# Performance work log

Hardware: AMD Instinct MI355X
Metric: run time of the kernel (lower is better)

Reference implementation:

```python
import jax, jax.numpy as jnp
import numpy as np

K, T, F = 12000, 35, 7          # voxels, points-per-voxel (cfg.VOXEL_POINT_COUNT), point feature dim
B, D, H, W = 1, 10, 400, 352    # scatter grid: [batch, depth, cfg.INPUT_HEIGHT, cfg.INPUT_WIDTH]
C_OUT = 128
EPS = 1e-3                      # Keras BatchNormalization default epsilon


def setup_inputs() -> dict:
    key = jax.random.key(0)
    ks = jax.random.split(key, 20)
    # point features, with per-voxel padding (points beyond count are zero)
    feat = jax.random.normal(ks[0], (K, T, F), dtype=jnp.float32)
    counts = jax.random.randint(ks[1], (K,), 1, T + 1)
    valid = (jnp.arange(T)[None, :] < counts[:, None]).astype(jnp.float32)  # [K,T]
    feat = feat * valid[:, :, None]
    # voxel coordinates: (batch, d, h, w), in-range per dimension
    c0 = jax.random.randint(ks[2], (K,), 0, B)
    c1 = jax.random.randint(ks[3], (K,), 0, D)
    c2 = jax.random.randint(ks[4], (K,), 0, H)
    c3 = jax.random.randint(ks[5], (K,), 0, W)
    coordinate = jnp.stack([c0, c1, c2, c3], axis=1).astype(jnp.int32)  # [K,4]
    p = lambda i, shape: jax.random.normal(ks[i], shape, dtype=jnp.float32) * 0.1
    return {
        "input_feature": feat,
        "w1": p(6, (F, 16)), "b1": p(7, (16,)),
        "gamma1": 1.0 + p(8, (16,)), "beta1": p(9, (16,)),
        "mean1": p(10, (16,)), "var1": jax.random.uniform(ks[11], (16,), minval=0.5, maxval=1.5),
        "w2": p(12, (32, 64)), "b2": p(13, (64,)),
        "gamma2": 1.0 + p(14, (64,)), "beta2": p(15, (64,)),
        "mean2": p(16, (64,)), "var2": jax.random.uniform(ks[17], (64,), minval=0.5, maxval=1.5),
        "coordinate": coordinate,
        "batch_size": B,
    }


def vfe(x, mask, w, b, gamma, beta, mean, var):
    # Dense + relu (per point), inference BatchNorm, max-aggregate, tile-concat, mask
    dense = jax.nn.relu(jnp.einsum('ktf,fu->ktu', x, w) + b)
    pw = gamma * (dense - mean) * jax.lax.rsqrt(var + EPS) + beta  # [K,T,U]
    agg = jnp.max(pw, axis=1, keepdims=True)                       # [K,1,U]
    cat = jnp.concatenate([pw, jnp.broadcast_to(agg, pw.shape)], axis=2)  # [K,T,2U]
    return cat * mask


def reference(input_feature, w1, b1, gamma1, beta1, mean1, var1,
              w2, b2, gamma2, beta2, mean2, var2, coordinate, batch_size):
    # mask: point is valid if max over its features != 0
    mask = (jnp.max(input_feature, axis=2, keepdims=True) != 0).astype(input_feature.dtype)
    x = vfe(input_feature, mask, w1, b1, gamma1, beta1, mean1, var1)   # [K,T,32]
    x = vfe(x, mask, w2, b2, gamma2, beta2, mean2, var2)               # [K,T,128]
    voxelwise = jnp.max(x, axis=1)                                     # [K,128]
    out = jnp.zeros((batch_size, D, H, W, C_OUT), dtype=voxelwise.dtype)
    # tf.scatter_nd semantics: duplicate indices accumulate (add)
    out = out.at[coordinate[:, 0], coordinate[:, 1], coordinate[:, 2], coordinate[:, 3]].add(voxelwise)
    return out
```

## Files before the change

kernel.cpp:

```cpp
#include <hip/hip_runtime.h>

#define KVOX 12000
#define TPTS 35
#define FIN  7
#define DD   10
#define HH   400
#define WW   352
#define CO   128
#define EPSBN 1e-3f
#define NCELL (DD * HH * WW)
#define CELLS_PER_BLK 8

__global__ __launch_bounds__(64) void vfe_compute(
    const float* __restrict__ feat,
    const float* __restrict__ w1, const float* __restrict__ b1,
    const float* __restrict__ g1, const float* __restrict__ be1,
    const float* __restrict__ m1, const float* __restrict__ v1,
    const float* __restrict__ w2, const float* __restrict__ b2,
    const float* __restrict__ g2, const float* __restrict__ be2,
    const float* __restrict__ m2, const float* __restrict__ v2,
    const int* __restrict__ coord,
    float* __restrict__ vox,
    int* __restrict__ head,
    int* __restrict__ nxt)
{
    const int k   = blockIdx.x;
    const int tid = threadIdx.x;

    __shared__ float sx[TPTS][FIN];
    __shared__ float smask[TPTS];
    __shared__ __align__(16) float sx2[TPTS][32];

    const float* fk = feat + (size_t)k * (TPTS * FIN);
    for (int i = tid; i < TPTS * FIN; i += 64)
        ((float*)sx)[i] = fk[i];
    __syncthreads();

    bool pred = false;
    if (tid < TPTS) {
        float mx = sx[tid][0];
        #pragma unroll
        for (int f = 1; f < FIN; ++f) mx = fmaxf(mx, sx[tid][f]);
        pred = (mx != 0.0f);
        smask[tid] = pred ? 1.0f : 0.0f;
    }
    unsigned long long bal = __ballot(pred);
    const int nvalid = __popcll(bal);
    __syncthreads();

    if (tid < 16) {
        const int u = tid;
        float w1c[FIN];
        #pragma unroll
        for (int f = 0; f < FIN; ++f) w1c[f] = w1[f * 16 + u];
        const float b     = b1[u];
        const float scale = g1[u] * rsqrtf(v1[u] + EPSBN);
        const float shift = be1[u] - m1[u] * scale;

        float agg = -INFINITY;
        float pw[TPTS];
        #pragma unroll
        for (int t = 0; t < TPTS; ++t) {
            float d = b;
            #pragma unroll
            for (int f = 0; f < FIN; ++f) d = fmaf(sx[t][f], w1c[f], d);
            d = fmaxf(d, 0.0f);
            float p = fmaf(d, scale, shift);
            agg = fmaxf(agg, p);
            pw[t] = p;
        }
        #pragma unroll
        for (int t = 0; t < TPTS; ++t) {
            const float mk = smask[t];
            sx2[t][u]      = pw[t] * mk;
            sx2[t][16 + u] = agg   * mk;
        }
    }
    __syncthreads();

    {
        const int v = tid;
        float w2c[32];
        #pragma unroll
        for (int u = 0; u < 32; ++u) w2c[u] = w2[u * 64 + v];
        const float b     = b2[v];
        const float scale = g2[v] * rsqrtf(v2[v] + EPSBN);
        const float shift = be2[v] - m2[v] * scale;

        float aggAll = -INFINITY;
        float voxA   = -INFINITY;
        #pragma unroll 5
        for (int t = 0; t < TPTS; ++t) {
            float d = b;
            const float4* xr = (const float4*)(&sx2[t][0]);
            #pragma unroll
            for (int q = 0; q < 8; ++q) {
                float4 xv = xr[q];
                d = fmaf(xv.x, w2c[4 * q + 0], d);
                d = fmaf(xv.y, w2c[4 * q + 1], d);
                d = fmaf(xv.z, w2c[4 * q + 2], d);
                d = fmaf(xv.w, w2c[4 * q + 3], d);
            }
            d = fmaxf(d, 0.0f);
            float p = fmaf(d, scale, shift);
            aggAll = fmaxf(aggAll, p);
            voxA   = fmaxf(voxA, p * smask[t]);
        }
        float voxB;
        if (nvalid == 0)          voxB = 0.0f;
        else if (nvalid < TPTS)   voxB = fmaxf(aggAll, 0.0f);
        else                      voxB = aggAll;

        float* vk = vox + (size_t)k * CO;
        vk[v]      = voxA;
        vk[64 + v] = voxB;

        if (v == 0) {
            const int4 c = ((const int4*)coord)[k];
            const int loc = (((c.x * DD + c.y) * HH + c.z) * WW + c.w);
            nxt[k] = atomicExch(&head[loc], k);
        }
    }
}

__global__ __launch_bounds__(256) void gather_out(
    const float* __restrict__ vox, const int* __restrict__ head,
    const int* __restrict__ nxt, float* __restrict__ out)
{
    const int tid  = threadIdx.x;
    const int cell = blockIdx.x * CELLS_PER_BLK + (tid >> 5);
    const int lane = tid & 31;

    float4 acc = make_float4(0.f, 0.f, 0.f, 0.f);
    int s = head[cell];
    while (s >= 0) {
        const float4 v = ((const float4*)vox)[s * 32 + lane];
        acc.x += v.x; acc.y += v.y; acc.z += v.z; acc.w += v.w;
        s = nxt[s];
    }
    ((float4*)out)[(size_t)cell * 32 + lane] = acc;
}

__global__ __launch_bounds__(64) void vfe_scatter_atomic(
    const float* __restrict__ feat,
    const float* __restrict__ w1, const float* __restrict__ b1,
    const float* __restrict__ g1, const float* __restrict__ be1,
    const float* __restrict__ m1, const float* __restrict__ v1,
    const float* __restrict__ w2, const float* __restrict__ b2,
    const float* __restrict__ g2, const float* __restrict__ be2,
    const float* __restrict__ m2, const float* __restrict__ v2,
    const int* __restrict__ coord,
    float* __restrict__ out)
{
    const int k   = blockIdx.x;
    const int tid = threadIdx.x;
    __shared__ float sx[TPTS][FIN];
    __shared__ float smask[TPTS];
    __shared__ __align__(16) float sx2[TPTS][32];
    const float* fk = feat + (size_t)k * (TPTS * FIN);
    for (int i = tid; i < TPTS * FIN; i += 64) ((float*)sx)[i] = fk[i];
    __syncthreads();
    bool pred = false;
    if (tid < TPTS) {
        float mx = sx[tid][0];
        #pragma unroll
        for (int f = 1; f < FIN; ++f) mx = fmaxf(mx, sx[tid][f]);
        pred = (mx != 0.0f);
        smask[tid] = pred ? 1.0f : 0.0f;
    }
    unsigned long long bal = __ballot(pred);
    const int nvalid = __popcll(bal);
    __syncthreads();
    if (tid < 16) {
        const int u = tid;
        float w1c[FIN];
        #pragma unroll
        for (int f = 0; f < FIN; ++f) w1c[f] = w1[f * 16 + u];
        const float b = b1[u];
        const float scale = g1[u] * rsqrtf(v1[u] + EPSBN);
        const float shift = be1[u] - m1[u] * scale;
        float agg = -INFINITY;
        float pw[TPTS];
        #pragma unroll
        for (int t = 0; t < TPTS; ++t) {
            float d = b;
            #pragma unroll
            for (int f = 0; f < FIN; ++f) d = fmaf(sx[t][f], w1c[f], d);
            d = fmaxf(d, 0.0f);
            float p = fmaf(d, scale, shift);
            agg = fmaxf(agg, p);
            pw[t] = p;
        }
        #pragma unroll
        for (int t = 0; t < TPTS; ++t) {
            const float mk = smask[t];
            sx2[t][u] = pw[t] * mk;
            sx2[t][16 + u] = agg * mk;
        }
    }
    __syncthreads();
    {
        const int v = tid;
        float w2c[32];
        #pragma unroll
        for (int u = 0; u < 32; ++u) w2c[u] = w2[u * 64 + v];
        const float b = b2[v];
        const float scale = g2[v] * rsqrtf(v2[v] + EPSBN);
        const float shift = be2[v] - m2[v] * scale;
        float aggAll = -INFINITY, voxA = -INFINITY;
        #pragma unroll 5
        for (int t = 0; t < TPTS; ++t) {
            float d = b;
            const float4* xr = (const float4*)(&sx2[t][0]);
            #pragma unroll
            for (int q = 0; q < 8; ++q) {
                float4 xv = xr[q];
                d = fmaf(xv.x, w2c[4 * q + 0], d);
                d = fmaf(xv.y, w2c[4 * q + 1], d);
                d = fmaf(xv.z, w2c[4 * q + 2], d);
                d = fmaf(xv.w, w2c[4 * q + 3], d);
            }
            d = fmaxf(d, 0.0f);
            float p = fmaf(d, scale, shift);
            aggAll = fmaxf(aggAll, p);
            voxA = fmaxf(voxA, p * smask[t]);
        }
        float voxB;
        if (nvalid == 0) voxB = 0.0f;
        else if (nvalid < TPTS) voxB = fmaxf(aggAll, 0.0f);
        else voxB = aggAll;
        const int4 c = ((const int4*)coord)[k];
        const int loc = (((c.x * DD + c.y) * HH + c.z) * WW + c.w);
        float* o = out + (size_t)loc * CO;
        atomicAdd(o + v, voxA);
        atomicAdd(o + 64 + v, voxB);
    }
}

extern "C" void kernel_launch(void* const* d_in, const int* in_sizes, int n_in,
                              void* d_out, int out_size, void* d_ws, size_t ws_size,
                              hipStream_t stream) {
    const float* feat = (const float*)d_in[0];
    const float* w1   = (const float*)d_in[1];
    const float* b1   = (const float*)d_in[2];
    const float* g1   = (const float*)d_in[3];
    const float* be1  = (const float*)d_in[4];
    const float* m1   = (const float*)d_in[5];
    const float* v1   = (const float*)d_in[6];
    const float* w2   = (const float*)d_in[7];
    const float* b2   = (const float*)d_in[8];
    const float* g2   = (const float*)d_in[9];
    const float* be2  = (const float*)d_in[10];
    const float* m2   = (const float*)d_in[11];
    const float* v2   = (const float*)d_in[12];
    const int*   coord = (const int*)d_in[13];
    float* out = (float*)d_out;

    const size_t voxB  = (size_t)KVOX * CO * sizeof(float);
    const size_t headB = (size_t)NCELL * sizeof(int);
    const size_t nxtB  = (size_t)KVOX * sizeof(int);
    const size_t need  = voxB + headB + nxtB;

    if (ws_size >= need) {
        float* vox = (float*)d_ws;
        int*   head = (int*)((char*)d_ws + voxB);
        int*   nxt  = (int*)((char*)d_ws + voxB + headB);

        hipMemsetAsync(head, 0xFF, headB, stream);
        vfe_compute<<<KVOX, 64, 0, stream>>>(feat, w1, b1, g1, be1, m1, v1,
                                             w2, b2, g2, be2, m2, v2, coord,
                                             vox, head, nxt);
        gather_out<<<NCELL / CELLS_PER_BLK, 256, 0, stream>>>(vox, head, nxt, out);
    } else {
        hipMemsetAsync(d_out, 0, (size_t)out_size * sizeof(float), stream);
        vfe_scatter_atomic<<<KVOX, 64, 0, stream>>>(feat, w1, b1, g1, be1, m1, v1,
                                                    w2, b2, g2, be2, m2, v2, coord, out);
    }
}
```

Before: 795.1 us.

## Fuse output zero-fill with VFE compute and replace linked-list gather with atomic scatter

The separate head-array memset and linked-list gather pass over every output cell are removed. The output zero-fill now runs inside the VFE compute kernel, whose blocks hold four voxels each and alternate between filling before or after their compute so the fill and compute overlap. A second small kernel then scatters voxel features into the output with per-channel atomic adds. This drops the head and next workspace and the gather pass's pointer chasing, at the cost of one large 180MB fill plus atomic contention on any duplicate cells.

```diff
diff --git a/kernel.cpp b/kernel.cpp
--- a/kernel.cpp
+++ b/kernel.cpp
@@ -9,9 +9,11 @@
 #define CO   128
 #define EPSBN 1e-3f
 #define NCELL (DD * HH * WW)
-#define CELLS_PER_BLK 8
-
-__global__ __launch_bounds__(64) void vfe_compute(
+#define CB    3000
+#define TOTALF4 ((size_t)NCELL * 32)
+#define SB    1500
+
+__global__ __launch_bounds__(256) void fused_fill_compute(
     const float* __restrict__ feat,
     const float* __restrict__ w1, const float* __restrict__ b1,
     const float* __restrict__ g1, const float* __restrict__ be1,
@@ -19,126 +21,132 @@
     const float* __restrict__ w2, const float* __restrict__ b2,
     const float* __restrict__ g2, const float* __restrict__ be2,
     const float* __restrict__ m2, const float* __restrict__ v2,
-    const int* __restrict__ coord,
     float* __restrict__ vox,
-    int* __restrict__ head,
-    int* __restrict__ nxt)
-{
-    const int k   = blockIdx.x;
-    const int tid = threadIdx.x;
-
-    __shared__ float sx[TPTS][FIN];
-    __shared__ float smask[TPTS];
-    __shared__ __align__(16) float sx2[TPTS][32];
-
-    const float* fk = feat + (size_t)k * (TPTS * FIN);
-    for (int i = tid; i < TPTS * FIN; i += 64)
-        ((float*)sx)[i] = fk[i];
-    __syncthreads();
-
-    bool pred = false;
-    if (tid < TPTS) {
-        float mx = sx[tid][0];
-        #pragma unroll
-        for (int f = 1; f < FIN; ++f) mx = fmaxf(mx, sx[tid][f]);
-        pred = (mx != 0.0f);
-        smask[tid] = pred ? 1.0f : 0.0f;
-    }
-    unsigned long long bal = __ballot(pred);
-    const int nvalid = __popcll(bal);
-    __syncthreads();
-
-    if (tid < 16) {
-        const int u = tid;
-        float w1c[FIN];
-        #pragma unroll
-        for (int f = 0; f < FIN; ++f) w1c[f] = w1[f * 16 + u];
-        const float b     = b1[u];
-        const float scale = g1[u] * rsqrtf(v1[u] + EPSBN);
-        const float shift = be1[u] - m1[u] * scale;
-
-        float agg = -INFINITY;
-        float pw[TPTS];
-        #pragma unroll
-        for (int t = 0; t < TPTS; ++t) {
-            float d = b;
-            #pragma unroll
-            for (int f = 0; f < FIN; ++f) d = fmaf(sx[t][f], w1c[f], d);
-            d = fmaxf(d, 0.0f);
-            float p = fmaf(d, scale, shift);
-            agg = fmaxf(agg, p);
-            pw[t] = p;
-        }
-        #pragma unroll
-        for (int t = 0; t < TPTS; ++t) {
-            const float mk = smask[t];
-            sx2[t][u]      = pw[t] * mk;
-            sx2[t][16 + u] = agg   * mk;
-        }
-    }
-    __syncthreads();
-
-    {
-        const int v = tid;
-        float w2c[32];
-        #pragma unroll
-        for (int u = 0; u < 32; ++u) w2c[u] = w2[u * 64 + v];
-        const float b     = b2[v];
-        const float scale = g2[v] * rsqrtf(v2[v] + EPSBN);
-        const float shift = be2[v] - m2[v] * scale;
-
-        float aggAll = -INFINITY;
-        float voxA   = -INFINITY;
-        #pragma unroll 5
-        for (int t = 0; t < TPTS; ++t) {
-            float d = b;
-            const float4* xr = (const float4*)(&sx2[t][0]);
-            #pragma unroll
-            for (int q = 0; q < 8; ++q) {
-                float4 xv = xr[q];
-                d = fmaf(xv.x, w2c[4 * q + 0], d);
-                d = fmaf(xv.y, w2c[4 * q + 1], d);
-                d = fmaf(xv.z, w2c[4 * q + 2], d);
-                d = fmaf(xv.w, w2c[4 * q + 3], d);
-            }
-            d = fmaxf(d, 0.0f);
-            float p = fmaf(d, scale, shift);
-            aggAll = fmaxf(aggAll, p);
-            voxA   = fmaxf(voxA, p * smask[t]);
-        }
-        float voxB;
-        if (nvalid == 0)          voxB = 0.0f;
-        else if (nvalid < TPTS)   voxB = fmaxf(aggAll, 0.0f);
-        else                      voxB = aggAll;
-
-        float* vk = vox + (size_t)k * CO;
-        vk[v]      = voxA;
-        vk[64 + v] = voxB;
-
-        if (v == 0) {
-            const int4 c = ((const int4*)coord)[k];
-            const int loc = (((c.x * DD + c.y) * HH + c.z) * WW + c.w);
-            nxt[k] = atomicExch(&head[loc], k);
-        }
-    }
-}
-
-__global__ __launch_bounds__(256) void gather_out(
-    const float* __restrict__ vox, const int* __restrict__ head,
-    const int* __restrict__ nxt, float* __restrict__ out)
+    float* __restrict__ out)
 {
     const int tid  = threadIdx.x;
-    const int cell = blockIdx.x * CELLS_PER_BLK + (tid >> 5);
-    const int lane = tid & 31;
-
-    float4 acc = make_float4(0.f, 0.f, 0.f, 0.f);
-    int s = head[cell];
-    while (s >= 0) {
-        const float4 v = ((const float4*)vox)[s * 32 + lane];
-        acc.x += v.x; acc.y += v.y; acc.z += v.z; acc.w += v.w;
-        s = nxt[s];
-    }
-    ((float4*)out)[(size_t)cell * 32 + lane] = acc;
+    const int wv   = tid >> 6;
+    const int lane = tid & 63;
+    const int k    = blockIdx.x * 4 + wv;
+
+    __shared__ float sx[4][TPTS][FIN];
+    __shared__ float smask[4][TPTS];
+    __shared__ __align__(16) float sx2[4][TPTS][32];
+
+    const bool fillFirst = (blockIdx.x & 1);
+
+    auto do_fill = [&]() {
+        const float4 z = make_float4(0.f, 0.f, 0.f, 0.f);
+        float4* o4 = (float4*)out;
+        const size_t stride = (size_t)CB * 256;
+        for (size_t i = (size_t)blockIdx.x * 256 + tid; i < TOTALF4; i += stride)
+            o4[i] = z;
+    };
+
+    if (fillFirst) do_fill();
+
+    {
+        const float* fk = feat + (size_t)k * (TPTS * FIN);
+        for (int i = lane; i < TPTS * FIN; i += 64)
+            ((float*)sx[wv])[i] = fk[i];
+        __syncthreads();
+
+        bool pred = false;
+        if (lane < TPTS) {
+            float mx = sx[wv][lane][0];
+            #pragma unroll
+            for (int f = 1; f < FIN; ++f) mx = fmaxf(mx, sx[wv][lane][f]);
+            pred = (mx != 0.0f);
+            smask[wv][lane] = pred ? 1.0f : 0.0f;
+        }
+        unsigned long long bal = __ballot(pred);
+        const int nvalid = __popcll(bal);
+        __syncthreads();
+
+        if (lane < 16) {
+            const int u = lane;
+            float w1c[FIN];
+            #pragma unroll
+            for (int f = 0; f < FIN; ++f) w1c[f] = w1[f * 16 + u];
+            const float b     = b1[u];
+            const float scale = g1[u] * rsqrtf(v1[u] + EPSBN);
+            const float shift = be1[u] - m1[u] * scale;
+
+            float agg = -INFINITY;
+            float pw[TPTS];
+            #pragma unroll
+            for (int t = 0; t < TPTS; ++t) {
+                float d = b;
+                #pragma unroll
+                for (int f = 0; f < FIN; ++f) d = fmaf(sx[wv][t][f], w1c[f], d);
+                d = fmaxf(d, 0.0f);
+                float p = fmaf(d, scale, shift);
+                agg = fmaxf(agg, p);
+                pw[t] = p;
+            }
+            #pragma unroll
+            for (int t = 0; t < TPTS; ++t) {
+                const float mk = smask[wv][t];
+                sx2[wv][t][u]      = pw[t] * mk;
+                sx2[wv][t][16 + u] = agg   * mk;
+            }
+        }
+        __syncthreads();
+
+        {
+            const int v = lane;
+            float w2c[32];
+            #pragma unroll
+            for (int u = 0; u < 32; ++u) w2c[u] = w2[u * 64 + v];
+            const float b     = b2[v];
+            const float scale = g2[v] * rsqrtf(v2[v] + EPSBN);
+            const float shift = be2[v] - m2[v] * scale;
+
+            float aggAll = -INFINITY;
+            float voxA   = -INFINITY;
+            #pragma unroll 5
+            for (int t = 0; t < TPTS; ++t) {
+                float d = b;
+                const float4* xr = (const float4*)(&sx2[wv][t][0]);
+                #pragma unroll
+                for (int q = 0; q < 8; ++q) {
+                    float4 xv = xr[q];
+                    d = fmaf(xv.x, w2c[4 * q + 0], d);
+                    d = fmaf(xv.y, w2c[4 * q + 1], d);
+                    d = fmaf(xv.z, w2c[4 * q + 2], d);
+                    d = fmaf(xv.w, w2c[4 * q + 3], d);
+                }
+                d = fmaxf(d, 0.0f);
+                float p = fmaf(d, scale, shift);
+                aggAll = fmaxf(aggAll, p);
+                voxA   = fmaxf(voxA, p * smask[wv][t]);
+            }
+            float voxB;
+            if (nvalid == 0)          voxB = 0.0f;
+            else if (nvalid < TPTS)   voxB = fmaxf(aggAll, 0.0f);
+            else                      voxB = aggAll;
+
+            float* vk = vox + (size_t)k * CO;
+            vk[v]      = voxA;
+            vk[64 + v] = voxB;
+        }
+    }
+
+    if (!fillFirst) do_fill();
+}
+
+__global__ __launch_bounds__(256) void scatter_add(
+    const float* __restrict__ vox, const int* __restrict__ coord,
+    float* __restrict__ out)
+{
+    const int stride = SB * 256;
+    for (int i = blockIdx.x * 256 + threadIdx.x; i < KVOX * CO; i += stride) {
+        const int k  = i >> 7;
+        const int ch = i & (CO - 1);
+        const int4 c = ((const int4*)coord)[k];
+        const int loc = (((c.x * DD + c.y) * HH + c.z) * WW + c.w);
+        atomicAdd(out + (size_t)loc * CO + ch, vox[i]);
+    }
 }
 
 __global__ __launch_bounds__(64) void vfe_scatter_atomic(
@@ -256,21 +264,14 @@
     const int*   coord = (const int*)d_in[13];
     float* out = (float*)d_out;
 
-    const size_t voxB  = (size_t)KVOX * CO * sizeof(float);
-    const size_t headB = (size_t)NCELL * sizeof(int);
-    const size_t nxtB  = (size_t)KVOX * sizeof(int);
-    const size_t need  = voxB + headB + nxtB;
-
-    if (ws_size >= need) {
+    const size_t voxB = (size_t)KVOX * CO * sizeof(float);
+
+    if (ws_size >= voxB) {
         float* vox = (float*)d_ws;
-        int*   head = (int*)((char*)d_ws + voxB);
-        int*   nxt  = (int*)((char*)d_ws + voxB + headB);
-
-        hipMemsetAsync(head, 0xFF, headB, stream);
-        vfe_compute<<<KVOX, 64, 0, stream>>>(feat, w1, b1, g1, be1, m1, v1,
-                                             w2, b2, g2, be2, m2, v2, coord,
-                                             vox, head, nxt);
-        gather_out<<<NCELL / CELLS_PER_BLK, 256, 0, stream>>>(vox, head, nxt, out);
+        fused_fill_compute<<<CB, 256, 0, stream>>>(feat, w1, b1, g1, be1, m1, v1,
+                                                   w2, b2, g2, be2, m2, v2,
+                                                   vox, out);
+        scatter_add<<<SB, 256, 0, stream>>>(vox, coord, out);
     } else {
         hipMemsetAsync(d_out, 0, (size_t)out_size * sizeof(float), stream);
         vfe_scatter_atomic<<<KVOX, 64, 0, stream>>>(feat, w1, b1, g1, be1, m1, v1,
```

Measured after the change: 757.3 us. 1.05x faster.
